# Kernel optimization log

Hardware: AMD Instinct MI355X
Metric: run time of the kernel (lower is better)

Reference implementation:

```python
import jax, jax.numpy as jnp
import numpy as np

B, N, K = 128, 131072, 256


def setup_inputs() -> dict:
    key = jax.random.key(0)
    k1, k2 = jax.random.split(key)
    score = jax.random.normal(k1, (B, N), dtype=jnp.float32)
    roi = jax.random.uniform(k2, (B, N, 4), dtype=jnp.float32)
    return {"score": score, "roi": roi, "k": K}


def reference(score, roi, k):
    # top-k over the anchor dim, sorted descending (matches tf.nn.top_k sorted=True)
    top_k_score, top_k_index = jax.lax.top_k(score, k)  # [B, k], [B, k]
    # gather ROI rows: equivalent of tf.gather_nd with (batch_idx, anchor_idx)
    roi_selected = jnp.take_along_axis(roi, top_k_index[:, :, None], axis=1)  # [B, k, 4]
    return roi_selected, top_k_score
```

## Files before the change

### kernel.cpp

```cpp
#include <hip/hip_runtime.h>
#include <stdint.h>


#define BATCH   128
#define NANCH   131072
#define KSEL    256
#define SPLITS  8
#define CHUNK   (NANCH / SPLITS)
#define TPB     256
#define V4PT    (CHUNK / TPB / 4)
#define NBUCK   4096
#define CAPMAX  8192
#define SORTCAP 2048
#define TPB2    512
#define RPT2    (CAPMAX / TPB2)

typedef unsigned long long ull;

__device__ __forceinline__ unsigned ord_of(float f) {
    unsigned u = __float_as_uint(f);
    return (u & 0x80000000u) ? ~u : (u | 0x80000000u);
}
__device__ __forceinline__ float f_of_ord(unsigned o) {
    unsigned u = (o & 0x80000000u) ? (o ^ 0x80000000u) : ~o;
    return __uint_as_float(u);
}

__device__ __forceinline__ int wave_incl_prefix(int v, int lane) {
#pragma unroll
    for (int off = 1; off < 64; off <<= 1) {
        int n = __shfl_up(v, off);
        if (lane >= off) v += n;
    }
    return v;
}
__device__ __forceinline__ int wave_incl_suffix(int v, int lane) {
#pragma unroll
    for (int off = 1; off < 64; off <<= 1) {
        int n = __shfl_down(v, off);
        if (lane + off < 64) v += n;
    }
    return v;
}

__global__ __launch_bounds__(TPB) void topk_stage1(
    const float* __restrict__ score, ull* __restrict__ cand,
    int* __restrict__ cnt, int cap)
{
    __shared__ int hist[NBUCK];
    __shared__ int wtot[TPB / 64];
    __shared__ int s_bstar;
    __shared__ int s_base;

    const int t    = threadIdx.x;
    const int lane = t & 63;
    const int wid  = t >> 6;
    const int sp   = blockIdx.x;
    const int b    = blockIdx.y;

    const float4* src = (const float4*)(score + (size_t)b * NANCH + (size_t)sp * CHUNK);
    float4 v[V4PT];
#pragma unroll
    for (int i = 0; i < V4PT; ++i) v[i] = src[i * TPB + t];

    for (int i = t; i < NBUCK; i += TPB) hist[i] = 0;
    __syncthreads();

#pragma unroll
    for (int i = 0; i < V4PT; ++i) {
        atomicAdd(&hist[ord_of(v[i].x) >> 20], 1);
        atomicAdd(&hist[ord_of(v[i].y) >> 20], 1);
        atomicAdd(&hist[ord_of(v[i].z) >> 20], 1);
        atomicAdd(&hist[ord_of(v[i].w) >> 20], 1);
    }
    __syncthreads();

    int ps = 0;
#pragma unroll
    for (int p = 0; p < 16; ++p) ps += hist[t * 16 + p];
    int sfx = wave_incl_suffix(ps, lane);
    if (lane == 0) wtot[wid] = sfx;
    __syncthreads();
    int hi = 0;
#pragma unroll
    for (int w = 0; w < TPB / 64; ++w) if (w > wid) hi += wtot[w];
    const int sinc = sfx + hi;

    {
        int running = sinc - ps;
#pragma unroll
        for (int p = 15; p >= 0; --p) {
            int nr = running + hist[t * 16 + p];
            if (nr >= KSEL && running < KSEL) s_bstar = t * 16 + p;
            running = nr;
        }
    }
    __syncthreads();
    const unsigned thr = (unsigned)s_bstar << 20;

    int qc = 0;
#pragma unroll
    for (int i = 0; i < V4PT; ++i) {
        qc += (ord_of(v[i].x) >= thr);
        qc += (ord_of(v[i].y) >= thr);
        qc += (ord_of(v[i].z) >= thr);
        qc += (ord_of(v[i].w) >= thr);
    }
    int pfx = wave_incl_prefix(qc, lane);
    if (lane == 63) wtot[wid] = pfx;
    __syncthreads();
    int lo = 0, total = 0;
#pragma unroll
    for (int w = 0; w < TPB / 64; ++w) {
        total += wtot[w];
        if (w < wid) lo += wtot[w];
    }
    if (t == 0) s_base = atomicAdd(&cnt[b], total);
    __syncthreads();

    int pos = s_base + lo + pfx - qc;
    ull* cb = cand + (size_t)b * cap;
    const int nbase = sp * CHUNK;
#pragma unroll
    for (int i = 0; i < V4PT; ++i) {
        const int n0 = nbase + 4 * (i * TPB + t);
        unsigned o;
        o = ord_of(v[i].x);
        if (o >= thr && pos < cap) { cb[pos++] = ((ull)o << 32) | (unsigned)(NANCH - 1 - n0); }
        o = ord_of(v[i].y);
        if (o >= thr && pos < cap) { cb[pos++] = ((ull)o << 32) | (unsigned)(NANCH - 2 - n0); }
        o = ord_of(v[i].z);
        if (o >= thr && pos < cap) { cb[pos++] = ((ull)o << 32) | (unsigned)(NANCH - 3 - n0); }
        o = ord_of(v[i].w);
        if (o >= thr && pos < cap) { cb[pos++] = ((ull)o << 32) | (unsigned)(NANCH - 4 - n0); }
    }
}

__global__ __launch_bounds__(TPB2) void topk_stage2(
    const ull* __restrict__ cand, const int* __restrict__ cnt,
    const float* __restrict__ roi, float* __restrict__ out_roi,
    float* __restrict__ out_score, int cap)
{
    __shared__ int hist[NBUCK];
    __shared__ int wtot[TPB2 / 64];
    __shared__ ull buf[SORTCAP];
    __shared__ int s_bstar, s_csel;

    const int t    = threadIdx.x;
    const int lane = t & 63;
    const int wid  = t >> 6;
    const int b    = blockIdx.x;
    const int c    = min(cnt[b], cap);
    const ull* cb  = cand + (size_t)b * cap;

    ull rk[RPT2];
#pragma unroll
    for (int q = 0; q < RPT2; ++q) {
        const int i = t + q * TPB2;
        rk[q] = (i < c) ? cb[i] : 0;
    }

    for (int i = t; i < NBUCK; i += TPB2) hist[i] = 0;
    if (t == 0) s_csel = 0;
    __syncthreads();
#pragma unroll
    for (int q = 0; q < RPT2; ++q) {
        if (t + q * TPB2 < c) atomicAdd(&hist[(unsigned)(rk[q] >> 52)], 1);
    }
    __syncthreads();

    const int G = NBUCK / TPB2;
    int ps = 0;
#pragma unroll
    for (int p = 0; p < G; ++p) ps += hist[t * G + p];
    int sfx = wave_incl_suffix(ps, lane);
    if (lane == 0) wtot[wid] = sfx;
    __syncthreads();
    int hi = 0;
#pragma unroll
    for (int w = 0; w < TPB2 / 64; ++w) if (w > wid) hi += wtot[w];
    const int sinc = sfx + hi;
    {
        int running = sinc - ps;
#pragma unroll
        for (int p = G - 1; p >= 0; --p) {
            int nr = running + hist[t * G + p];
            if (nr >= KSEL && running < KSEL) s_bstar = t * G + p;
            running = nr;
        }
    }
    __syncthreads();
    const unsigned bstar = (unsigned)s_bstar;

#pragma unroll
    for (int q = 0; q < RPT2; ++q) {
        if (t + q * TPB2 < c && (unsigned)(rk[q] >> 52) >= bstar) {
            int p = atomicAdd(&s_csel, 1);
            if (p < SORTCAP) buf[p] = rk[q];
        }
    }
    __syncthreads();
    const int C = min(s_csel, SORTCAP);
    int P = KSEL;
    while (P < C) P <<= 1;
    for (int i = C + t; i < P; i += TPB2) buf[i] = 0;
    __syncthreads();

    for (int kk = 2; kk <= P; kk <<= 1) {
        for (int j = kk >> 1; j > 0; j >>= 1) {
            for (int i = t; i < P; i += TPB2) {
                int ixj = i ^ j;
                if (ixj > i) {
                    ull a = buf[i], d = buf[ixj];
                    bool up = (i & kk) == 0;
                    bool sw = up ? (a < d) : (a > d);
                    if (sw) { buf[i] = d; buf[ixj] = a; }
                }
            }
            __syncthreads();
        }
    }

    if (t < KSEL) {
        ull k = buf[t];
        int idx = NANCH - 1 - (int)(unsigned)(k & 0xffffffffull);
        float4 r = ((const float4*)roi)[(size_t)b * NANCH + idx];
        ((float4*)out_roi)[b * KSEL + t] = r;
    } else if (t < 2 * KSEL) {
        const int tt = t - KSEL;
        ull k = buf[tt];
        out_score[b * KSEL + tt] = f_of_ord((unsigned)(k >> 32));
    }
}

extern "C" void kernel_launch(void* const* d_in, const int* in_sizes, int n_in,
                              void* d_out, int out_size, void* d_ws, size_t ws_size,
                              hipStream_t stream)
{
    const float* score = (const float*)d_in[0];
    const float* roi   = (const float*)d_in[1];
    float* out_roi   = (float*)d_out;
    float* out_score = (float*)d_out + (size_t)BATCH * KSEL * 4;

    int* cnt  = (int*)d_ws;
    ull* cand = (ull*)((char*)d_ws + 4096);
    long long avail = ((long long)ws_size - 4096) / (long long)(sizeof(ull) * BATCH);
    int cap = (int)avail;
    if (cap > CAPMAX) cap = CAPMAX;
    if (cap < 1) cap = 1;

    hipMemsetAsync(cnt, 0, BATCH * sizeof(int), stream);
    topk_stage1<<<dim3(SPLITS, BATCH), TPB, 0, stream>>>(score, cand, cnt, cap);
    topk_stage2<<<BATCH, TPB2, 0, stream>>>(cand, cnt, roi, out_roi, out_score, cap);
}
```

Baseline: 360.3 us.

## Use per-split candidate segments, drop memset and atomics, double split count

Stage 1 now writes each block's candidates into a fixed per-(batch,split) segment with its own count, so the global atomicAdd and the memset launch go away. Splits double to 16, which halves the per-thread register tile and raises block count for occupancy. Stage 2 reads the per-split segments directly. Scores are converted to ordered keys once and kept in registers. Risk: candidates beyond SEGCAP per split are silently dropped, which could matter if one split holds many top values. It also assumes the workspace is large enough with no size check.

```diff
diff --git a/kernel.cpp b/kernel.cpp
--- a/kernel.cpp
+++ b/kernel.cpp
@@ -5,15 +5,15 @@
 #define BATCH   128
 #define NANCH   131072
 #define KSEL    256
-#define SPLITS  8
+#define SPLITS  16
 #define CHUNK   (NANCH / SPLITS)
 #define TPB     256
 #define V4PT    (CHUNK / TPB / 4)
 #define NBUCK   4096
 #define CAPMAX  8192
+#define SEGCAP  (CAPMAX / SPLITS)
 #define SORTCAP 2048
 #define TPB2    512
-#define RPT2    (CAPMAX / TPB2)
 
 typedef unsigned long long ull;
 
@@ -45,12 +45,11 @@
 
 __global__ __launch_bounds__(TPB) void topk_stage1(
     const float* __restrict__ score, ull* __restrict__ cand,
-    int* __restrict__ cnt, int cap)
+    int* __restrict__ cnt)
 {
     __shared__ int hist[NBUCK];
     __shared__ int wtot[TPB / 64];
     __shared__ int s_bstar;
-    __shared__ int s_base;
 
     const int t    = threadIdx.x;
     const int lane = t & 63;
@@ -59,19 +58,23 @@
     const int b    = blockIdx.y;
 
     const float4* src = (const float4*)(score + (size_t)b * NANCH + (size_t)sp * CHUNK);
-    float4 v[V4PT];
-#pragma unroll
-    for (int i = 0; i < V4PT; ++i) v[i] = src[i * TPB + t];
-
-    for (int i = t; i < NBUCK; i += TPB) hist[i] = 0;
-    __syncthreads();
-
-#pragma unroll
-    for (int i = 0; i < V4PT; ++i) {
-        atomicAdd(&hist[ord_of(v[i].x) >> 20], 1);
-        atomicAdd(&hist[ord_of(v[i].y) >> 20], 1);
-        atomicAdd(&hist[ord_of(v[i].z) >> 20], 1);
-        atomicAdd(&hist[ord_of(v[i].w) >> 20], 1);
+    uint4 v[V4PT];
+#pragma unroll
+    for (int i = 0; i < V4PT; ++i) {
+        float4 f = src[i * TPB + t];
+        v[i].x = ord_of(f.x); v[i].y = ord_of(f.y);
+        v[i].z = ord_of(f.z); v[i].w = ord_of(f.w);
+    }
+
+    for (int i = t; i < NBUCK / 4; i += TPB) ((int4*)hist)[i] = make_int4(0, 0, 0, 0);
+    __syncthreads();
+
+#pragma unroll
+    for (int i = 0; i < V4PT; ++i) {
+        atomicAdd(&hist[v[i].x >> 20], 1);
+        atomicAdd(&hist[v[i].y >> 20], 1);
+        atomicAdd(&hist[v[i].z >> 20], 1);
+        atomicAdd(&hist[v[i].w >> 20], 1);
     }
     __syncthreads();
 
@@ -101,10 +104,10 @@
     int qc = 0;
 #pragma unroll
     for (int i = 0; i < V4PT; ++i) {
-        qc += (ord_of(v[i].x) >= thr);
-        qc += (ord_of(v[i].y) >= thr);
-        qc += (ord_of(v[i].z) >= thr);
-        qc += (ord_of(v[i].w) >= thr);
+        qc += (v[i].x >= thr);
+        qc += (v[i].y >= thr);
+        qc += (v[i].z >= thr);
+        qc += (v[i].w >= thr);
     }
     int pfx = wave_incl_prefix(qc, lane);
     if (lane == 63) wtot[wid] = pfx;
@@ -115,31 +118,30 @@
         total += wtot[w];
         if (w < wid) lo += wtot[w];
     }
-    if (t == 0) s_base = atomicAdd(&cnt[b], total);
-    __syncthreads();
-
-    int pos = s_base + lo + pfx - qc;
-    ull* cb = cand + (size_t)b * cap;
+    if (t == 0) cnt[b * SPLITS + sp] = (total < SEGCAP) ? total : SEGCAP;
+
+    int pos = lo + pfx - qc;
+    ull* cb = cand + (size_t)b * CAPMAX + (size_t)sp * SEGCAP;
     const int nbase = sp * CHUNK;
 #pragma unroll
     for (int i = 0; i < V4PT; ++i) {
         const int n0 = nbase + 4 * (i * TPB + t);
         unsigned o;
-        o = ord_of(v[i].x);
-        if (o >= thr && pos < cap) { cb[pos++] = ((ull)o << 32) | (unsigned)(NANCH - 1 - n0); }
-        o = ord_of(v[i].y);
-        if (o >= thr && pos < cap) { cb[pos++] = ((ull)o << 32) | (unsigned)(NANCH - 2 - n0); }
-        o = ord_of(v[i].z);
-        if (o >= thr && pos < cap) { cb[pos++] = ((ull)o << 32) | (unsigned)(NANCH - 3 - n0); }
-        o = ord_of(v[i].w);
-        if (o >= thr && pos < cap) { cb[pos++] = ((ull)o << 32) | (unsigned)(NANCH - 4 - n0); }
+        o = v[i].x;
+        if (o >= thr && pos < SEGCAP) { cb[pos++] = ((ull)o << 32) | (unsigned)(NANCH - 1 - n0); }
+        o = v[i].y;
+        if (o >= thr && pos < SEGCAP) { cb[pos++] = ((ull)o << 32) | (unsigned)(NANCH - 2 - n0); }
+        o = v[i].z;
+        if (o >= thr && pos < SEGCAP) { cb[pos++] = ((ull)o << 32) | (unsigned)(NANCH - 3 - n0); }
+        o = v[i].w;
+        if (o >= thr && pos < SEGCAP) { cb[pos++] = ((ull)o << 32) | (unsigned)(NANCH - 4 - n0); }
     }
 }
 
 __global__ __launch_bounds__(TPB2) void topk_stage2(
     const ull* __restrict__ cand, const int* __restrict__ cnt,
     const float* __restrict__ roi, float* __restrict__ out_roi,
-    float* __restrict__ out_score, int cap)
+    float* __restrict__ out_score)
 {
     __shared__ int hist[NBUCK];
     __shared__ int wtot[TPB2 / 64];
@@ -150,22 +152,23 @@
     const int lane = t & 63;
     const int wid  = t >> 6;
     const int b    = blockIdx.x;
-    const int c    = min(cnt[b], cap);
-    const ull* cb  = cand + (size_t)b * cap;
-
-    ull rk[RPT2];
-#pragma unroll
-    for (int q = 0; q < RPT2; ++q) {
-        const int i = t + q * TPB2;
-        rk[q] = (i < c) ? cb[i] : 0;
-    }
-
-    for (int i = t; i < NBUCK; i += TPB2) hist[i] = 0;
+    const ull* cb  = cand + (size_t)b * CAPMAX;
+
+    int csp[SPLITS];
+    ull rk[SPLITS];
+#pragma unroll
+    for (int sp = 0; sp < SPLITS; ++sp) {
+        int c = cnt[b * SPLITS + sp];
+        csp[sp] = (c < SEGCAP) ? c : SEGCAP;
+        rk[sp] = (t < csp[sp]) ? cb[sp * SEGCAP + t] : 0;
+    }
+
+    for (int i = t; i < NBUCK / 4; i += TPB2) ((int4*)hist)[i] = make_int4(0, 0, 0, 0);
     if (t == 0) s_csel = 0;
     __syncthreads();
 #pragma unroll
-    for (int q = 0; q < RPT2; ++q) {
-        if (t + q * TPB2 < c) atomicAdd(&hist[(unsigned)(rk[q] >> 52)], 1);
+    for (int sp = 0; sp < SPLITS; ++sp) {
+        if (t < csp[sp]) atomicAdd(&hist[(unsigned)(rk[sp] >> 52)], 1);
     }
     __syncthreads();
 
@@ -193,10 +196,10 @@
     const unsigned bstar = (unsigned)s_bstar;
 
 #pragma unroll
-    for (int q = 0; q < RPT2; ++q) {
-        if (t + q * TPB2 < c && (unsigned)(rk[q] >> 52) >= bstar) {
+    for (int sp = 0; sp < SPLITS; ++sp) {
+        if (t < csp[sp] && (unsigned)(rk[sp] >> 52) >= bstar) {
             int p = atomicAdd(&s_csel, 1);
-            if (p < SORTCAP) buf[p] = rk[q];
+            if (p < SORTCAP) buf[p] = rk[sp];
         }
     }
     __syncthreads();
@@ -243,13 +246,8 @@
     float* out_score = (float*)d_out + (size_t)BATCH * KSEL * 4;
 
     int* cnt  = (int*)d_ws;
-    ull* cand = (ull*)((char*)d_ws + 4096);
-    long long avail = ((long long)ws_size - 4096) / (long long)(sizeof(ull) * BATCH);
-    int cap = (int)avail;
-    if (cap > CAPMAX) cap = CAPMAX;
-    if (cap < 1) cap = 1;
-
-    hipMemsetAsync(cnt, 0, BATCH * sizeof(int), stream);
-    topk_stage1<<<dim3(SPLITS, BATCH), TPB, 0, stream>>>(score, cand, cnt, cap);
-    topk_stage2<<<BATCH, TPB2, 0, stream>>>(cand, cnt, roi, out_roi, out_score, cap);
-}
+    ull* cand = (ull*)((char*)d_ws + 8192);
+
+    topk_stage1<<<dim3(SPLITS, BATCH), TPB, 0, stream>>>(score, cand, cnt);
+    topk_stage2<<<BATCH, TPB2, 0, stream>>>(cand, cnt, roi, out_roi, out_score);
+}
```

Result: no change. 356.4 us (-1.1%).
